# Optimization experiments

Measured on AMD Instinct MI355X. Metric: run time of the kernel, lower is better.

Reference implementation:

```python
import jax, jax.numpy as jnp
import numpy as np

K = 5          # kernel_size per dim
B = 100        # batch size (hard-coded in source)
GRID = 28
NUM_FIRST_FC = 49  # adjs[2].size(0) = 7*7


def spline_conv(x, edge_index, pseudo, W, root, bias):
    """Degree-1 open B-spline graph conv (SplineGCN).
    x: [N, Cin]; edge_index: [2, E] (src, dst); pseudo: [E, 2] in [0,1];
    W: [K*K, Cin, Cout]; root: [Cin, Cout]; bias: [Cout].
    out_i = mean_{j->i} sum_taps b_tap(u_ij) * (x_j @ W[k_tap]) + x_i @ root + bias
    """
    N = x.shape[0]
    src, dst = edge_index[0], edge_index[1]
    pos = pseudo * (K - 1)                     # open spline: scale to [0, K-1]
    kf = jnp.floor(pos)
    frac = pos - kf                            # [E, 2]
    k0 = kf.astype(jnp.int32)
    k1 = jnp.minimum(k0 + 1, K - 1)
    # Precompute x @ W[k] for all 25 kernel indices: [N, K*K, Cout]
    y = jnp.einsum('ni,kio->nko', x, W)
    fx, fy = frac[:, 0], frac[:, 1]
    taps = [
        (k0[:, 0], k0[:, 1], (1 - fx) * (1 - fy)),
        (k0[:, 0], k1[:, 1], (1 - fx) * fy),
        (k1[:, 0], k0[:, 1], fx * (1 - fy)),
        (k1[:, 0], k1[:, 1], fx * fy),
    ]
    msg = jnp.zeros((src.shape[0], W.shape[2]), dtype=x.dtype)
    for ax, ay, w in taps:
        msg = msg + w[:, None] * y[src, ax * K + ay]   # gather [E, Cout]
    agg = jax.ops.segment_sum(msg, dst, num_segments=N)
    deg = jax.ops.segment_sum(jnp.ones_like(msg[:, 0]), dst, num_segments=N)
    return agg / jnp.maximum(deg, 1.0)[:, None] + x @ root + bias


def max_pool2(x):  # x: [b, H, W, C] -> [b, H/2, W/2, C] (same math as NCHW pool)
    b, h, w, c = x.shape
    return x.reshape(b, h // 2, 2, w // 2, 2, c).max(axis=(2, 4))


def setup_inputs() -> dict:
    key = jax.random.key(0)
    ks = jax.random.split(key, 16)
    N0, N1 = B * GRID * GRID, B * (GRID // 2) * (GRID // 2)
    E0, E1 = N0 * 8, N1 * 8
    s = 0.1
    return {
        'x': jax.random.normal(ks[0], (N0, 1), dtype=jnp.float32),
        'pseudo0': jax.random.uniform(ks[1], (E0, 2), dtype=jnp.float32),
        'pseudo1': jax.random.uniform(ks[2], (E1, 2), dtype=jnp.float32),
        'W1': jax.random.normal(ks[3], (K * K, 1, 32), dtype=jnp.float32) * s,
        'root1': jax.random.normal(ks[4], (1, 32), dtype=jnp.float32) * s,
        'b1': jnp.zeros((32,), dtype=jnp.float32),
        'W2': jax.random.normal(ks[5], (K * K, 32, 64), dtype=jnp.float32) * s,
        'root2': jax.random.normal(ks[6], (32, 64), dtype=jnp.float32) * s,
        'b2': jnp.zeros((64,), dtype=jnp.float32),
        'fc1_w': jax.random.normal(ks[7], (NUM_FIRST_FC * 64, 512), dtype=jnp.float32) * 0.02,
        'fc1_b': jnp.zeros((512,), dtype=jnp.float32),
        'fc2_w': jax.random.normal(ks[8], (512, 10), dtype=jnp.float32) * 0.02,
        'fc2_b': jnp.zeros((10,), dtype=jnp.float32),
        'edge_index0': jax.random.randint(ks[9], (2, E0), 0, N0, dtype=jnp.int32),
        'edge_index1': jax.random.randint(ks[10], (2, E1), 0, N1, dtype=jnp.int32),
    }


def reference(x, pseudo0, pseudo1, W1, root1, b1, W2, root2, b2,
              fc1_w, fc1_b, fc2_w, fc2_b, edge_index0, edge_index1):
    elu = jax.nn.elu
    # conv1 on 28x28 grid graph
    h = elu(spline_conv(x, edge_index0, pseudo0, W1, root1, b1))   # [B*784, 32]
    h = h.reshape(-1, GRID, GRID, 32)                              # [B, 28, 28, 32]
    h = max_pool2(h)                                               # [B, 14, 14, 32]
    h = h.reshape(-1, 32)                                          # [B*196, 32]
    # conv2 on 14x14 grid graph
    h = elu(spline_conv(h, edge_index1, pseudo1, W2, root2, b2))   # [B*196, 64]
    # faithful replication of the source's reshapes: (B*196) rows -> (B/4, 28, 28, 64)
    h = h.reshape(-1, GRID, GRID, 64)                              # [25, 28, 28, 64]
    h = max_pool2(h)                                               # [25, 14, 14, 64]
    h = h.reshape(-1, NUM_FIRST_FC * 64)                           # [100, 3136]
    h = elu(h @ fc1_w + fc1_b)
    # F.dropout with training=False (eval) is identity
    h = elu(h @ fc2_w + fc2_b)
    return jax.nn.log_softmax(h, axis=-1)
```

## Files before the change

kernel.cpp:

```cpp
#include <hip/hip_runtime.h>
#include <hip/hip_bf16.h>

#define KK 5
constexpr int N0 = 78400;
constexpr int E0 = 627200;
constexpr int N1 = 19600;
constexpr int E1 = 156800;
constexpr int C1 = 32, C2 = 64;
constexpr int BSZ = 100;
constexpr int FC1_IN = 3136, FC1_OUT = 512;
constexpr int KEXT = 832;
constexpr int ULS = 836;
constexpr int UBS = 856;
constexpr int KZ = 7;

constexpr int NB0 = 1400;
constexpr int CAP0 = 576;
constexpr int NB1 = 1225;
constexpr int CAP1 = 224;
constexpr int NBT = NB0 + NB1;

constexpr float SC1  = 4194304.f;
constexpr float ISC1 = 1.f / 4194304.f;
constexpr float SC2  = 1048576.f;
constexpr float ISC2 = 1.f / 1048576.f;

typedef __attribute__((ext_vector_type(8))) short bf16x8;
typedef __attribute__((ext_vector_type(4))) float f32x4;

__device__ __forceinline__ unsigned short f2bf(float f) {
    union { float f; unsigned u; } v; v.f = f;
    unsigned u = v.u;
    unsigned r = (u + 0x7FFF + ((u >> 16) & 1)) >> 16;
    return (unsigned short)r;
}

__device__ __forceinline__ void taps4(float px, float py,
                                      int& a00, int& a01, int& a10, int& a11,
                                      float& fx, float& fy) {
    float kfx = floorf(px), kfy = floorf(py);
    fx = px - kfx; fy = py - kfy;
    int k0x = min(max((int)kfx, 0), KK - 1);
    int k0y = min(max((int)kfy, 0), KK - 1);
    int k1x = min(k0x + 1, KK - 1), k1y = min(k0y + 1, KK - 1);
    a00 = k0x * KK + k0y; a01 = k0x * KK + k1y;
    a10 = k1x * KK + k0y; a11 = k1x * KK + k1y;
}

__global__ void coarse_bin(const int* __restrict__ ei0, const int* __restrict__ ei1,
                           const float* __restrict__ ps0, const float* __restrict__ ps1,
                           int* __restrict__ gcur,
                           int2* __restrict__ pk0, int2* __restrict__ pk1,
                           const float* __restrict__ fc1w, const float* __restrict__ W2,
                           const float* __restrict__ root2,
                           unsigned short* __restrict__ wt1,
                           unsigned short* __restrict__ w2t) {
    __shared__ int hist[NBT];
    __shared__ int gbase[NBT];
    __shared__ unsigned short tile[64 * 66];
    int t = threadIdx.x;
    if (blockIdx.x >= 192) {
        int pb = blockIdx.x - 192;
        if (pb >= 392) {
            int base = (pb - 392) * 6656;
            for (int i2 = t; i2 < 6656; i2 += 512) {
                int idx = base + i2;
                int o = idx / KEXT, k = idx - o * KEXT;
                float v = (k < 800) ? W2[k * 64 + o] : root2[(k - 800) * 64 + o];
                w2t[idx] = f2bf(v);
            }
            return;
        }
        int k0 = (pb >> 3) * 64, j0 = (pb & 7) * 64;
        int jj = t & 63, ks = t >> 6;
        for (int kk = ks; kk < 64; kk += 8)
            tile[kk * 66 + jj] = f2bf(fc1w[(k0 + kk) * FC1_OUT + j0 + jj]);
        __syncthreads();
        int kk2 = t & 63, js = t >> 6;
        for (int j2 = js; j2 < 64; j2 += 8)
            wt1[(j0 + j2) * FC1_IN + k0 + kk2] = tile[kk2 * 66 + j2];
        return;
    }
    for (int i = t; i < NBT; i += 512) hist[i] = 0;
    __syncthreads();
    int e0b = blockIdx.x * 4096;
    int keys[8], rnk[8], pay0[8], pay1[8];
#pragma unroll
    for (int j = 0; j < 8; j++) {
        int e = e0b + t + j * 512;
        int k = -1, p0 = 0, p1v = 0;
        if (e < E0) {
            int dst = ei0[E0 + e];
            int b = dst / 56, low = dst - b * 56;
            k = b;
            float px = ps0[2 * e] * 4.f, py = ps0[2 * e + 1] * 4.f;
            unsigned ux = min((unsigned)(px * 16384.f + 0.5f), 65535u);
            unsigned uy = min((unsigned)(py * 16384.f + 0.5f), 65535u);
            p0 = ei0[e] | (low << 20); p1v = (int)(ux | (uy << 16));
        } else if (e < E0 + E1) {
            int el = e - E0;
            int dst = ei1[E1 + el];
            k = NB0 + (dst >> 4);
            float px = ps1[2 * el] * 4.f, py = ps1[2 * el + 1] * 4.f;
            unsigned ux = min((unsigned)(px * 16384.f + 0.5f), 65535u);
            unsigned uy = min((unsigned)(py * 16384.f + 0.5f), 65535u);
            p0 = ei1[el] | ((dst & 15) << 20); p1v = (int)(ux | (uy << 16));
        }
        keys[j] = k; pay0[j] = p0; pay1[j] = p1v;
    }
#pragma unroll
    for (int j = 0; j < 8; j++)
        if (keys[j] >= 0) rnk[j] = atomicAdd(&hist[keys[j]], 1);
    __syncthreads();
    for (int i = t; i < NBT; i += 512)
        gbase[i] = hist[i] ? atomicAdd(&gcur[i], hist[i]) : 0;
    __syncthreads();
#pragma unroll
    for (int j = 0; j < 8; j++) {
        if (keys[j] >= 0) {
            int k = keys[j];
            int p = gbase[k] + rnk[j];
            if (k < NB0) {
                if (p < CAP0) pk0[k * CAP0 + p] = make_int2(pay0[j], pay1[j]);
            } else {
                if (p < CAP1) pk1[(k - NB0) * CAP1 + p] = make_int2(pay0[j], pay1[j]);
            }
        }
    }
}

__global__ __launch_bounds__(256, 4)
void conv1_pool(const int2* __restrict__ pk0, const int* __restrict__ cnt0,
                const float* __restrict__ x,
                const float* __restrict__ W1,
                const float* __restrict__ root, const float* __restrict__ bias,
                float* __restrict__ p1) {
    __shared__ int   Ui[56 * 26];
    __shared__ float h1t[56 * 32];
    int t = threadIdx.x;
    int bb = blockIdx.x;
    int n0 = bb * 56;
    for (int i = t; i < 56 * 26; i += 256) Ui[i] = 0;
    __syncthreads();
    int cnt = min(cnt0[bb], CAP0);
    const int2* bkt = pk0 + bb * CAP0;
    for (int j = t; j < cnt; j += 256) {
        int2 r = bkt[j];
        int src = r.x & 0xFFFFF, low = (r.x >> 20) & 63;
        float px = (float)((unsigned)r.y & 0xFFFF) * (1.f / 16384.f);
        float py = (float)((unsigned)r.y >> 16) * (1.f / 16384.f);
        int a00, a01, a10, a11; float fx, fy;
        taps4(px, py, a00, a01, a10, a11, fx, fy);
        float xv = x[src];
        float gx = 1.f - fx, gy = 1.f - fy;
        int* row = Ui + low * 26;
        atomicAdd(row + a00, __float2int_rn(gx * gy * xv * SC1));
        atomicAdd(row + a01, __float2int_rn(gx * fy * xv * SC1));
        atomicAdd(row + a10, __float2int_rn(fx * gy * xv * SC1));
        atomicAdd(row + a11, __float2int_rn(fx * fy * xv * SC1));
        atomicAdd(row + 25, 1);
    }
    __syncthreads();
    {
        int o = t & 31, ng = t >> 5;
        float w1c[25];
#pragma unroll
        for (int a = 0; a < 25; a++) w1c[a] = W1[a * C1 + o];
        float ro = root[o], bo = bias[o];
        for (int j2 = 0; j2 < 7; j2++) {
            int nl = ng * 7 + j2;
            int n = n0 + nl;
            float acc = 0.f;
#pragma unroll
            for (int a = 0; a < 25; a++) acc += (float)Ui[nl * 26 + a] * w1c[a];
            float invd = ISC1 / fmaxf((float)Ui[nl * 26 + 25], 1.f);
            float v = acc * invd + x[n] * ro + bo;
            h1t[nl * 32 + o] = v > 0.f ? v : expm1f(v);
        }
    }
    __syncthreads();
    for (int i2 = t; i2 < 448; i2 += 256) {
        int o2 = i2 & 31, pc = i2 >> 5;
        float m0 = h1t[(2 * pc) * 32 + o2],      m1 = h1t[(2 * pc + 1) * 32 + o2];
        float m2 = h1t[(28 + 2 * pc) * 32 + o2], m3 = h1t[(28 + 2 * pc + 1) * 32 + o2];
        p1[(bb * 14 + pc) * C1 + o2] = fmaxf(fmaxf(m0, m1), fmaxf(m2, m3));
    }
}

__global__ __launch_bounds__(512, 2)
void conv2_fused(const float* __restrict__ p1, const int2* __restrict__ pk1,
                 const int* __restrict__ cnt1,
                 const unsigned short* __restrict__ w2t,
                 const float* __restrict__ b2, float* __restrict__ h2) {
    __shared__ int   Ui[16 * ULS];
    __shared__ int   es[CAP1];
    __shared__ int   et[CAP1];
    __shared__ float efx[CAP1], efy[CAP1];
    __shared__ int   degc[16];
    unsigned short* Ub = (unsigned short*)Ui;
    int t = threadIdx.x;
    int bx = blockIdx.x;
    int nb = bx * 16;
    int i = t & 31;
    int g = t >> 5;
    int* up = Ui + g * ULS;
#pragma unroll
    for (int a = 0; a < 25; a++) up[a * 32 + i] = 0;
    up[800 + i] = __float2int_rn(p1[(nb + g) * C1 + i] * SC2);
    if (t < 16) degc[t] = 0;
    __syncthreads();
    int cnt = min(cnt1[bx], CAP1);
    for (int j = t; j < cnt; j += 512) {
        int2 r = pk1[bx * CAP1 + j];
        es[j] = r.x;
        float px = (float)((unsigned)r.y & 0xFFFF) * (1.f / 16384.f);
        float py = (float)((unsigned)r.y >> 16) * (1.f / 16384.f);
        int a00, a01, a10, a11; float fx, fy;
        taps4(px, py, a00, a01, a10, a11, fx, fy);
        et[j] = a00 | (a01 << 5) | (a10 << 10) | (a11 << 15);
        efx[j] = fx; efy[j] = fy;
        atomicAdd(&degc[(r.x >> 20) & 15], 1);
    }
    __syncthreads();
    for (int j = g; j < cnt; j += 16) {
        int rx = es[j];
        float xv = p1[(rx & 0xFFFFF) * C1 + i];
        int* row = Ui + ((rx >> 20) & 15) * ULS;
        int m = et[j];
        float fx = efx[j], fy = efy[j];
        float gx = 1.f - fx, gy = 1.f - fy;
        atomicAdd(row + (m & 31) * 32 + i,         __float2int_rn(gx * gy * xv * SC2));
        atomicAdd(row + ((m >> 5) & 31) * 32 + i,  __float2int_rn(gx * fy * xv * SC2));
        atomicAdd(row + ((m >> 10) & 31) * 32 + i, __float2int_rn(fx * gy * xv * SC2));
        atomicAdd(row + ((m >> 15) & 31) * 32 + i, __float2int_rn(fx * fy * xv * SC2));
    }
    __syncthreads();
    {
        int g2 = t >> 5, i2c = t & 31;
        float invd = 1.f / fmaxf((float)degc[g2], 1.f);
        float stap = ISC2 * invd;
        const int* srcp = Ui + g2 * ULS + i2c * 26;
        float rv[26];
#pragma unroll
        for (int j = 0; j < 26; j++) {
            float v = (float)srcp[j];
            rv[j] = (i2c * 26 + j < 800) ? v * stap : v * ISC2;
        }
        __syncthreads();
        unsigned* dstp = (unsigned*)(Ub + g2 * UBS + i2c * 26);
#pragma unroll
        for (int j = 0; j < 13; j++) {
            unsigned lo = f2bf(rv[2 * j]), hi = f2bf(rv[2 * j + 1]);
            dstp[j] = lo | (hi << 16);
        }
    }
    __syncthreads();
    int wv = t >> 6, lane = t & 63, quad = lane >> 4, lrow = lane & 15;
    if (wv < 4) {
        f32x4 acc = {0.f, 0.f, 0.f, 0.f};
        const unsigned short* bbase = w2t + (wv * 16 + lrow) * KEXT;
        const unsigned short* abase = Ub + lrow * UBS;
#pragma unroll
        for (int kc = 0; kc < 26; kc++) {
            bf16x8 a = *(const bf16x8*)(abase + kc * 32 + quad * 8);
            bf16x8 b = *(const bf16x8*)(bbase + kc * 32 + quad * 8);
            acc = __builtin_amdgcn_mfma_f32_16x16x32_bf16(a, b, acc, 0, 0, 0);
        }
        int o = wv * 16 + lrow;
        float bo = b2[o];
#pragma unroll
        for (int r = 0; r < 4; r++) {
            int node = quad * 4 + r;
            float v = acc[r] + bo;
            v = v > 0.f ? v : expm1f(v);
            h2[(nb + node) * C2 + o] = v;
        }
    }
}

__global__ void pool2b(const float* __restrict__ h2, unsigned short* __restrict__ p2b) {
    int idx = blockIdx.x * blockDim.x + threadIdx.x;
    if (idx >= 112 * FC1_IN) return;
    if (idx >= 100 * FC1_IN) { p2b[idx] = 0; return; }
    int o = idx & 63; int t2 = idx >> 6;
    int c = t2 % 14; int r = (t2 / 14) % 14; int b = t2 / 196;
    const float* base = h2 + (((b * 28 + 2 * r) * 28 + 2 * c) * C2 + o);
    float m = fmaxf(fmaxf(base[0], base[C2]),
                    fmaxf(base[28 * C2], base[28 * C2 + C2]));
    p2b[idx] = f2bf(m);
}

__global__ void gemm_fc1(const unsigned short* __restrict__ p2b,
                         const unsigned short* __restrict__ wt1,
                         float* __restrict__ z1p) {
    constexpr int AS = 232;
    __shared__ unsigned short as_[16 * AS];
    int t = threadIdx.x;
    int jt = blockIdx.x, mt = blockIdx.y, kz = blockIdx.z;
    int wv = t >> 6, lane = t & 63, quad = lane >> 4, lrow = lane & 15;
    int m0 = mt * 16;
    int kbase = kz * 448;
    const unsigned short* bbase = wt1 + (jt * 64 + wv * 16 + lrow) * FC1_IN + kbase;
    f32x4 acc = {0.f, 0.f, 0.f, 0.f};
    for (int ch = 0; ch < 2; ch++) {
        __syncthreads();
        for (int slot = t; slot < 448; slot += 256) {
            int r = slot / 28, c = slot - (slot / 28) * 28;
            *(uint4*)(as_ + r * AS + c * 8) =
                *(const uint4*)(p2b + (m0 + r) * FC1_IN + kbase + ch * 224 + c * 8);
        }
        __syncthreads();
        const unsigned short* ab = as_ + lrow * AS;
        const unsigned short* bb = bbase + ch * 224;
#pragma unroll
        for (int kk = 0; kk < 7; kk++) {
            bf16x8 a = *(const bf16x8*)(ab + kk * 32 + quad * 8);
            bf16x8 b = *(const bf16x8*)(bb + kk * 32 + quad * 8);
            acc = __builtin_amdgcn_mfma_f32_16x16x32_bf16(a, b, acc, 0, 0, 0);
        }
    }
    int n = jt * 64 + wv * 16 + lrow;
#pragma unroll
    for (int r = 0; r < 4; r++) {
        int m = m0 + quad * 4 + r;
        z1p[kz * (112 * FC1_OUT) + m * FC1_OUT + n] = acc[r];
    }
}

__global__ void fc2_lsm(const float* __restrict__ z1p, const float* __restrict__ fc1b,
                        const float* __restrict__ w, const float* __restrict__ fc2b,
                        float* __restrict__ out) {
    int b = blockIdx.x;
    int t = threadIdx.x;
    int wv = t >> 6;
    int lane = t & 63;
    float acc = 0.f;
#pragma unroll
    for (int m = 0; m < 8; m++) {
        int k = lane * 8 + m;
        float xv = fc1b[k];
#pragma unroll
        for (int p = 0; p < KZ; p++)
            xv += z1p[p * (112 * FC1_OUT) + b * FC1_OUT + k];
        xv = xv > 0.f ? xv : expm1f(xv);
        acc += xv * w[k * 10 + wv];
    }
#pragma unroll
    for (int off = 32; off > 0; off >>= 1) acc += __shfl_down(acc, off);
    __shared__ float zs[10];
    if (lane == 0) {
        float z = acc + fc2b[wv];
        zs[wv] = z > 0.f ? z : expm1f(z);
    }
    __syncthreads();
    if (t < 10) {
        float m = -1e30f;
        for (int jj = 0; jj < 10; jj++) m = fmaxf(m, zs[jj]);
        float s = 0.f;
        for (int jj = 0; jj < 10; jj++) s += expf(zs[jj] - m);
        out[b * 10 + t] = zs[t] - m - logf(s);
    }
}

extern "C" void kernel_launch(void* const* d_in, const int* in_sizes, int n_in,
                              void* d_out, int out_size, void* d_ws, size_t ws_size,
                              hipStream_t stream) {
    const float* x     = (const float*)d_in[0];
    const float* ps0   = (const float*)d_in[1];
    const float* ps1   = (const float*)d_in[2];
    const float* W1    = (const float*)d_in[3];
    const float* root1 = (const float*)d_in[4];
    const float* b1    = (const float*)d_in[5];
    const float* W2    = (const float*)d_in[6];
    const float* root2 = (const float*)d_in[7];
    const float* b2v   = (const float*)d_in[8];
    const float* fc1w  = (const float*)d_in[9];
    const float* fc1b  = (const float*)d_in[10];
    const float* fc2w  = (const float*)d_in[11];
    const float* fc2b  = (const float*)d_in[12];
    const int*   ei0   = (const int*)d_in[13];
    const int*   ei1   = (const int*)d_in[14];

    float* ws = (float*)d_ws;
    int*  gcur = (int*)ws;
    int2* pk0  = (int2*)(ws + 2688);
    int2* pk1  = (int2*)(ws + 1615488);
    float* p1  = ws + 2164288;
    float* h2  = ws + 2791488;
    unsigned short* p2b = (unsigned short*)(ws + 4045888);
    float* z1p = ws + 4221504;
    unsigned short* w2t = (unsigned short*)(ws + 4622912);
    unsigned short* wt1 = (unsigned short*)(ws + 4649536);

    hipMemsetAsync(gcur, 0, (size_t)NBT * sizeof(int), stream);

    coarse_bin<<<592, 512, 0, stream>>>(ei0, ei1, ps0, ps1, gcur, pk0, pk1,
                                        fc1w, W2, root2, wt1, w2t);
    conv1_pool<<<NB0, 256, 0, stream>>>(pk0, gcur, x, W1, root1, b1, p1);
    conv2_fused<<<NB1, 512, 0, stream>>>(p1, pk1, gcur + NB0, w2t, b2v, h2);
    pool2b<<<(112 * FC1_IN + 255) / 256, 256, 0, stream>>>(h2, p2b);
    gemm_fc1<<<dim3(8, 7, KZ), 256, 0, stream>>>(p2b, wt1, z1p);
    fc2_lsm<<<BSZ, 640, 0, stream>>>(z1p, fc1b, fc2w, fc2b, (float*)d_out);
}
```

Baseline: 186.4 us.

## Fuse second max-pool into conv2 epilogue via ordered-float atomicMax

Removes the pool2b kernel and the h2 intermediate buffer. conv2_fused now writes each output straight into a pooled buffer with atomicMax on an order-preserving unsigned encoding of the float. gemm_fc1 decodes that buffer to bf16 while staging its A tile, and coarse_bin gains extra blocks that initialise the buffer. This saves one launch and a round trip of h2 through memory, at the cost of four-way atomic contention per pooled element and wider 32-bit reads in gemm_fc1. conv1_pool's launch bounds are also raised to target higher occupancy.

```diff
diff --git a/kernel.cpp b/kernel.cpp
--- a/kernel.cpp
+++ b/kernel.cpp
@@ -35,6 +35,15 @@
     return (unsigned short)r;
 }
 
+__device__ __forceinline__ unsigned fenc(float f) {
+    unsigned u = __float_as_uint(f);
+    return (u & 0x80000000u) ? ~u : (u | 0x80000000u);
+}
+__device__ __forceinline__ unsigned short fdec_bf(unsigned e) {
+    unsigned u = (e & 0x80000000u) ? (e & 0x7FFFFFFFu) : ~e;
+    return f2bf(__uint_as_float(u));
+}
+
 __device__ __forceinline__ void taps4(float px, float py,
                                       int& a00, int& a01, int& a10, int& a11,
                                       float& fx, float& fy) {
@@ -54,13 +63,20 @@
                            const float* __restrict__ fc1w, const float* __restrict__ W2,
                            const float* __restrict__ root2,
                            unsigned short* __restrict__ wt1,
-                           unsigned short* __restrict__ w2t) {
+                           unsigned short* __restrict__ w2t,
+                           unsigned* __restrict__ pmax) {
     __shared__ int hist[NBT];
     __shared__ int gbase[NBT];
     __shared__ unsigned short tile[64 * 66];
     int t = threadIdx.x;
     if (blockIdx.x >= 192) {
         int pb = blockIdx.x - 192;
+        if (pb >= 400) {
+            for (int idx = (pb - 400) * 512 + t; idx < 112 * FC1_IN; idx += 8 * 512)
+                pmax[idx] = (idx < 100 * FC1_IN) ? 0x007FFFFFu
+                                                 : 0x80000000u;
+            return;
+        }
         if (pb >= 392) {
             int base = (pb - 392) * 6656;
             for (int i2 = t; i2 < 6656; i2 += 512) {
@@ -129,7 +145,7 @@
     }
 }
 
-__global__ __launch_bounds__(256, 4)
+__global__ __launch_bounds__(256, 6)
 void conv1_pool(const int2* __restrict__ pk0, const int* __restrict__ cnt0,
                 const float* __restrict__ x,
                 const float* __restrict__ W1,
@@ -191,7 +207,7 @@
 void conv2_fused(const float* __restrict__ p1, const int2* __restrict__ pk1,
                  const int* __restrict__ cnt1,
                  const unsigned short* __restrict__ w2t,
-                 const float* __restrict__ b2, float* __restrict__ h2) {
+                 const float* __restrict__ b2, unsigned* __restrict__ pmax) {
     __shared__ int   Ui[16 * ULS];
     __shared__ int   es[CAP1];
     __shared__ int   et[CAP1];
@@ -273,24 +289,17 @@
             int node = quad * 4 + r;
             float v = acc[r] + bo;
             v = v > 0.f ? v : expm1f(v);
-            h2[(nb + node) * C2 + o] = v;
-        }
-    }
-}
-
-__global__ void pool2b(const float* __restrict__ h2, unsigned short* __restrict__ p2b) {
-    int idx = blockIdx.x * blockDim.x + threadIdx.x;
-    if (idx >= 112 * FC1_IN) return;
-    if (idx >= 100 * FC1_IN) { p2b[idx] = 0; return; }
-    int o = idx & 63; int t2 = idx >> 6;
-    int c = t2 % 14; int r = (t2 / 14) % 14; int b = t2 / 196;
-    const float* base = h2 + (((b * 28 + 2 * r) * 28 + 2 * c) * C2 + o);
-    float m = fmaxf(fmaxf(base[0], base[C2]),
-                    fmaxf(base[28 * C2], base[28 * C2 + C2]));
-    p2b[idx] = f2bf(m);
-}
-
-__global__ void gemm_fc1(const unsigned short* __restrict__ p2b,
+            int n1 = nb + node;
+            int b28 = n1 / 784;
+            int rem = n1 - b28 * 784;
+            int rr = rem / 28, cc = rem - rr * 28;
+            int flat = ((b28 * 14 + (rr >> 1)) * 14 + (cc >> 1)) * 64 + o;
+            atomicMax(&pmax[flat], fenc(v));
+        }
+    }
+}
+
+__global__ void gemm_fc1(const unsigned* __restrict__ pmax,
                          const unsigned short* __restrict__ wt1,
                          float* __restrict__ z1p) {
     constexpr int AS = 232;
@@ -306,8 +315,14 @@
         __syncthreads();
         for (int slot = t; slot < 448; slot += 256) {
             int r = slot / 28, c = slot - (slot / 28) * 28;
-            *(uint4*)(as_ + r * AS + c * 8) =
-                *(const uint4*)(p2b + (m0 + r) * FC1_IN + kbase + ch * 224 + c * 8);
+            const unsigned* gp = pmax + (m0 + r) * FC1_IN + kbase + ch * 224 + c * 8;
+            uint4 e0 = *(const uint4*)gp;
+            uint4 e1 = *(const uint4*)(gp + 4);
+            unsigned w0 = (unsigned)fdec_bf(e0.x) | ((unsigned)fdec_bf(e0.y) << 16);
+            unsigned w1 = (unsigned)fdec_bf(e0.z) | ((unsigned)fdec_bf(e0.w) << 16);
+            unsigned w2 = (unsigned)fdec_bf(e1.x) | ((unsigned)fdec_bf(e1.y) << 16);
+            unsigned w3 = (unsigned)fdec_bf(e1.z) | ((unsigned)fdec_bf(e1.w) << 16);
+            *(uint4*)(as_ + r * AS + c * 8) = make_uint4(w0, w1, w2, w3);
         }
         __syncthreads();
         const unsigned short* ab = as_ + lrow * AS;
@@ -386,19 +401,17 @@
     int2* pk0  = (int2*)(ws + 2688);
     int2* pk1  = (int2*)(ws + 1615488);
     float* p1  = ws + 2164288;
-    float* h2  = ws + 2791488;
-    unsigned short* p2b = (unsigned short*)(ws + 4045888);
-    float* z1p = ws + 4221504;
-    unsigned short* w2t = (unsigned short*)(ws + 4622912);
-    unsigned short* wt1 = (unsigned short*)(ws + 4649536);
+    unsigned* pmax = (unsigned*)(ws + 2791488);
+    float* z1p = ws + 3142720;
+    unsigned short* w2t = (unsigned short*)(ws + 3544128);
+    unsigned short* wt1 = (unsigned short*)(ws + 3570752);
 
     hipMemsetAsync(gcur, 0, (size_t)NBT * sizeof(int), stream);
 
-    coarse_bin<<<592, 512, 0, stream>>>(ei0, ei1, ps0, ps1, gcur, pk0, pk1,
-                                        fc1w, W2, root2, wt1, w2t);
+    coarse_bin<<<600, 512, 0, stream>>>(ei0, ei1, ps0, ps1, gcur, pk0, pk1,
+                                        fc1w, W2, root2, wt1, w2t, pmax);
     conv1_pool<<<NB0, 256, 0, stream>>>(pk0, gcur, x, W1, root1, b1, p1);
-    conv2_fused<<<NB1, 512, 0, stream>>>(p1, pk1, gcur + NB0, w2t, b2v, h2);
-    pool2b<<<(112 * FC1_IN + 255) / 256, 256, 0, stream>>>(h2, p2b);
-    gemm_fc1<<<dim3(8, 7, KZ), 256, 0, stream>>>(p2b, wt1, z1p);
+    conv2_fused<<<NB1, 512, 0, stream>>>(p1, pk1, gcur + NB0, w2t, b2v, pmax);
+    gemm_fc1<<<dim3(8, 7, KZ), 256, 0, stream>>>(pmax, wt1, z1p);
     fc2_lsm<<<BSZ, 640, 0, stream>>>(z1p, fc1b, fc2w, fc2b, (float*)d_out);
 }
```

Result: no change. 184.7 us (-0.9%).
